# Performance work log

Hardware: AMD Instinct MI355X
Metric: run time of the kernel (lower is better)

Reference implementation:

```python
import jax, jax.numpy as jnp
import numpy as np

DIM = 384
HEADS = 8


def setup_inputs() -> dict:
    key = jax.random.key(0)
    ks = jax.random.split(key, 6)
    B, H, W = 8, 64, 64
    N, C = H * W, DIM
    s = 0.02  # init scale for weights
    return {
        "x": jax.random.normal(ks[0], (B, N, C), jnp.float32),
        # depthwise conv: OIHW with feature_group_count=C -> [C,1,3,3]
        "w_sr": jax.random.normal(ks[1], (C, 1, 3, 3), jnp.float32) * s,
        "b_sr": jax.random.normal(ks[2], (C,), jnp.float32) * s,
        "ln_g": jnp.ones((C,), jnp.float32),
        "ln_b": jnp.zeros((C,), jnp.float32),
        # linears stored [in, out] (torch stores [out,in]; random so equivalent)
        "w_qkv": jax.random.normal(ks[3], (C, 3 * C), jnp.float32) * s,
        "w_proj": jax.random.normal(ks[4], (C, C), jnp.float32) * s,
        "b_proj": jax.random.normal(ks[5], (C,), jnp.float32) * s,
        "H": 64,
        "W": 64,
    }


def reference(x, w_sr, b_sr, ln_g, ln_b, w_qkv, w_proj, b_proj, H, W):
    B, N, C = x.shape
    h = HEADS
    d = C // h
    shortcut = x

    # --- depthwise conv branch: sr(x) -> LN -> GELU -> residual add ---
    x_img = x.transpose(0, 2, 1).reshape(B, C, H, W)
    x_sr = jax.lax.conv_general_dilated(
        x_img, w_sr, window_strides=(1, 1), padding="SAME",
        dimension_numbers=("NCHW", "OIHW", "NCHW"), feature_group_count=C,
    ) + b_sr[None, :, None, None]
    x_sr = x_sr.reshape(B, C, N).transpose(0, 2, 1)  # [B, N, C]
    mu = x_sr.mean(-1, keepdims=True)
    var = x_sr.var(-1, keepdims=True)
    xn = (x_sr - mu) * jax.lax.rsqrt(var + 1e-5) * ln_g + ln_b
    x = x + jax.nn.gelu(xn, approximate=False)  # torch GELU is erf-based

    # --- linear attention ---
    qkv = (x @ w_qkv).reshape(B, N, 3, h, d)
    q = qkv[:, :, 0].transpose(0, 2, 1, 3)  # [B, h, N, d]
    k = qkv[:, :, 1].transpose(0, 2, 1, 3)
    v = qkv[:, :, 2].transpose(0, 2, 1, 3)
    q = jax.nn.softmax(q, axis=-2)  # softmax over sequence dim N
    k = jax.nn.softmax(k, axis=-1)  # softmax over head_dim
    ctx = jnp.einsum("bhnd,bhne->bhde", k, v)          # [B, h, d, d]
    attn = jnp.einsum("bhnd,bhde->bhne", q, ctx)       # [B, h, N, d]
    attn = attn.transpose(0, 2, 1, 3).reshape(B, N, C)

    out = attn @ w_proj + b_proj
    return out + shortcut
```

## Files before the change

### kernel.cpp

```cpp
#include <hip/hip_runtime.h>

typedef unsigned short u16;
typedef u16   u16x4  __attribute__((ext_vector_type(4)));
typedef u16   u16x8  __attribute__((ext_vector_type(8)));
typedef short short8 __attribute__((ext_vector_type(8)));
typedef float floatx4 __attribute__((ext_vector_type(4)));
typedef float f4     __attribute__((ext_vector_type(4)));

#define BB 8
#define NN 4096
#define CC 384

__device__ __forceinline__ u16 f2bf(float f){
  unsigned u = __float_as_uint(f);
  u += 0x7FFFu + ((u >> 16) & 1u);
  return (u16)(u >> 16);
}

__global__ __launch_bounds__(256) void k_prep(const float* __restrict__ wqkv, u16* __restrict__ WT)
{
  const int cg = blockIdx.x % 18;
  const int kg = blockIdx.x / 18;
  const int c0 = cg << 6, k0 = kg << 6;
  const int tid = threadIdx.x;
  __shared__ u16 t[64][72];
#pragma unroll
  for (int i = 0; i < 4; i++) {
    int idx = tid + (i << 8);
    int r = idx >> 4, c4 = (idx & 15) << 2;
    f4 v = *(const f4*)(wqkv + (size_t)(k0 + r) * 1152 + c0 + c4);
#pragma unroll
    for (int j = 0; j < 4; j++) t[c4 + j][r] = f2bf(v[j]);
  }
  __syncthreads();
#pragma unroll
  for (int i = 0; i < 2; i++) {
    int idx = tid + (i << 8);
    int c = idx >> 3, j = (idx & 7) << 3;
    *(u16x8*)(WT + (size_t)(c0 + c) * 384 + k0 + j) = *(const u16x8*)&t[c][j];
  }
}

__global__ __launch_bounds__(384) void k_conv_ln_gelu(
    const float* __restrict__ x, const float* __restrict__ w_sr, const float* __restrict__ b_sr,
    const float* __restrict__ ln_g, const float* __restrict__ ln_b, u16* __restrict__ xa16)
{
  const int blk = blockIdx.x;
  const int b = blk >> 9;
  const int hh = (blk >> 3) & 63;
  const int ww0 = (blk & 7) << 3;
  const int c = threadIdx.x;

  float wgt[9];
#pragma unroll
  for (int i = 0; i < 9; i++) wgt[i] = w_sr[c * 9 + i];
  const float lg = ln_g[c], lb = ln_b[c];
  const float bias = b_sr[c];

  float rowv[3][10];
#pragma unroll
  for (int r = 0; r < 3; r++) {
    int y = hh + r - 1;
    bool yok = (unsigned)y < 64u;
#pragma unroll
    for (int j = 0; j < 10; j++) {
      int xx = ww0 + j - 1;
      bool ok = yok && ((unsigned)xx < 64u);
      rowv[r][j] = ok ? x[((size_t)((b << 12) + (y << 6) + xx)) * CC + c] : 0.f;
    }
  }

  float acc[8];
#pragma unroll
  for (int p = 0; p < 8; p++) {
    float a = bias;
#pragma unroll
    for (int r = 0; r < 3; r++)
#pragma unroll
      for (int j = 0; j < 3; j++)
        a += rowv[r][p + j] * wgt[r * 3 + j];
    acc[p] = a;
  }

  __shared__ float ls1[6][8], ls2[6][8], mb[2][8];
  const int wid = threadIdx.x >> 6, lane = threadIdx.x & 63;
#pragma unroll
  for (int p = 0; p < 8; p++) {
    float s1 = acc[p], s2 = acc[p] * acc[p];
#pragma unroll
    for (int o = 32; o > 0; o >>= 1) { s1 += __shfl_down(s1, o); s2 += __shfl_down(s2, o); }
    if (lane == 0) { ls1[wid][p] = s1; ls2[wid][p] = s2; }
  }
  __syncthreads();
  if (threadIdx.x < 8) {
    int p = threadIdx.x;
    float a = 0.f, q = 0.f;
#pragma unroll
    for (int i = 0; i < 6; i++) { a += ls1[i][p]; q += ls2[i][p]; }
    float mean = a * (1.0f / CC);
    float var  = q * (1.0f / CC) - mean * mean;
    mb[0][p] = mean; mb[1][p] = rsqrtf(var + 1e-5f);
  }
  __syncthreads();
#pragma unroll
  for (int p = 0; p < 8; p++) {
    float xn = (acc[p] - mb[0][p]) * mb[1][p] * lg + lb;
    float g  = 0.5f * xn * (1.0f + erff(xn * 0.70710678118654752f));
    size_t pix = (size_t)(b << 12) + (hh << 6) + ww0 + p;
    xa16[pix * CC + c] = f2bf(rowv[1][p + 1] + g);
  }
}


__global__ __launch_bounds__(512) void k_kv(
    const u16* __restrict__ xa16, const u16* __restrict__ WT,
    u16* __restrict__ K16T, u16* __restrict__ V16T)
{
  const int rt = blockIdx.x;
  const int g  = blockIdx.y;
  const int b  = rt >> 6;
  const int n0 = rt << 6;
  const int tid = threadIdx.x;
  const int wv = tid >> 6, lane = tid & 63, l15 = lane & 15, quad = lane >> 4;
  const int wc = wv;

  __shared__ __attribute__((aligned(16))) u16 lA[2][64][40];
  __shared__ __attribute__((aligned(16))) u16 lB[2][384][40];

  const u16* Bbase = WT + (size_t)(384 + g * 384) * 384;
  const int rA = tid >> 2, cA = (tid & 3) << 3;

  floatx4 acc[12];
  const floatx4 z = {0.f, 0.f, 0.f, 0.f};
#pragma unroll
  for (int i = 0; i < 12; i++) acc[i] = z;

  if (tid < 256)
    *(u16x8*)&lA[0][rA][cA] = *(const u16x8*)(xa16 + (size_t)(n0 + rA) * 384 + cA);
#pragma unroll
  for (int i = 0; i < 3; i++) {
    int idx = tid + (i << 9);
    *(u16x8*)&lB[0][idx >> 2][(idx & 3) << 3] = *(const u16x8*)(Bbase + (size_t)(idx >> 2) * 384 + ((idx & 3) << 3));
  }
  __syncthreads();

  for (int t = 0; t < 12; t++) {
    const int cur = t & 1, nxt = cur ^ 1;
    u16x8 ra, rb[3];
    const bool pf = (t < 11);
    const int kn = (t + 1) << 5;
    if (pf) {
      if (tid < 256) ra = *(const u16x8*)(xa16 + (size_t)(n0 + rA) * 384 + kn + cA);
#pragma unroll
      for (int i = 0; i < 3; i++) {
        int idx = tid + (i << 9);
        rb[i] = *(const u16x8*)(Bbase + (size_t)(idx >> 2) * 384 + kn + ((idx & 3) << 3));
      }
    }
    short8 af[4], bf[3];
#pragma unroll
    for (int mi = 0; mi < 4; mi++) af[mi] = *(const short8*)&lA[cur][(mi << 4) + l15][quad << 3];
#pragma unroll
    for (int ni = 0; ni < 3; ni++) bf[ni] = *(const short8*)&lB[cur][wc * 48 + (ni << 4) + l15][quad << 3];
#pragma unroll
    for (int mi = 0; mi < 4; mi++)
#pragma unroll
      for (int ni = 0; ni < 3; ni++)
        acc[mi * 3 + ni] = __builtin_amdgcn_mfma_f32_16x16x32_bf16(af[mi], bf[ni], acc[mi * 3 + ni], 0, 0, 0);
    if (pf) {
      if (tid < 256) *(u16x8*)&lA[nxt][rA][cA] = ra;
#pragma unroll
      for (int i = 0; i < 3; i++) {
        int idx = tid + (i << 9);
        *(u16x8*)&lB[nxt][idx >> 2][(idx & 3) << 3] = rb[i];
      }
    }
    __syncthreads();
  }

  if (g == 0) {
#pragma unroll
    for (int mi = 0; mi < 4; mi++)
#pragma unroll
      for (int rr = 0; rr < 4; rr++) {
        float x0 = acc[mi * 3 + 0][rr], x1 = acc[mi * 3 + 1][rr], x2 = acc[mi * 3 + 2][rr];
        float m = fmaxf(fmaxf(x0, x1), x2);
#pragma unroll
        for (int o = 8; o >= 1; o >>= 1) m = fmaxf(m, __shfl_xor(m, o));
        float e0 = expf(x0 - m), e1 = expf(x1 - m), e2 = expf(x2 - m);
        float s = e0 + e1 + e2;
#pragma unroll
        for (int o = 8; o >= 1; o >>= 1) s += __shfl_xor(s, o);
        float inv = 1.0f / s;
        acc[mi * 3 + 0][rr] = e0 * inv; acc[mi * 3 + 1][rr] = e1 * inv; acc[mi * 3 + 2][rr] = e2 * inv;
      }
  }

  u16* dst = g ? V16T : K16T;
  const int nl = ((rt & 63) << 6) + (quad << 2);
#pragma unroll
  for (int mi = 0; mi < 4; mi++)
#pragma unroll
    for (int ni = 0; ni < 3; ni++) {
      int hd = wc * 48 + (ni << 4) + l15;
      u16x4 v4 = { f2bf(acc[mi * 3 + ni][0]), f2bf(acc[mi * 3 + ni][1]),
                   f2bf(acc[mi * 3 + ni][2]), f2bf(acc[mi * 3 + ni][3]) };
      *(u16x4*)(dst + ((size_t)b * 384 + hd) * 4096 + nl + (mi << 4)) = v4;
    }
}

__global__ __launch_bounds__(512) void k_qps(
    const u16* __restrict__ xa16, const u16* __restrict__ WT, float* __restrict__ S,
    u16* __restrict__ P16)
{
  const int bm = blockIdx.x;
  const int b = bm >> 6;
  const int n0 = bm << 6;
  const int tid = threadIdx.x;
  const int wv = tid >> 6, lane = tid & 63, l15 = lane & 15, quad = lane >> 4;
  const int wc = wv;

  __shared__ __attribute__((aligned(16))) u16 lA[2][64][40];
  __shared__ __attribute__((aligned(16))) u16 lB[2][384][40];

  const u16* Bbase = WT;
  const int rA = tid >> 2, cA = (tid & 3) << 3;

  floatx4 acc[12];
  const floatx4 z = {0.f, 0.f, 0.f, 0.f};
#pragma unroll
  for (int i = 0; i < 12; i++) acc[i] = z;

  if (tid < 256)
    *(u16x8*)&lA[0][rA][cA] = *(const u16x8*)(xa16 + (size_t)(n0 + rA) * 384 + cA);
#pragma unroll
  for (int i = 0; i < 3; i++) {
    int idx = tid + (i << 9);
    *(u16x8*)&lB[0][idx >> 2][(idx & 3) << 3] = *(const u16x8*)(Bbase + (size_t)(idx >> 2) * 384 + ((idx & 3) << 3));
  }
  __syncthreads();

  for (int t = 0; t < 12; t++) {
    const int cur = t & 1, nxt = cur ^ 1;
    u16x8 ra, rb[3];
    const bool pf = (t < 11);
    const int kn = (t + 1) << 5;
    if (pf) {
      if (tid < 256) ra = *(const u16x8*)(xa16 + (size_t)(n0 + rA) * 384 + kn + cA);
#pragma unroll
      for (int i = 0; i < 3; i++) {
        int idx = tid + (i << 9);
        rb[i] = *(const u16x8*)(Bbase + (size_t)(idx >> 2) * 384 + kn + ((idx & 3) << 3));
      }
    }
    short8 af[4], bf[3];
#pragma unroll
    for (int mi = 0; mi < 4; mi++) af[mi] = *(const short8*)&lA[cur][(mi << 4) + l15][quad << 3];
#pragma unroll
    for (int ni = 0; ni < 3; ni++) bf[ni] = *(const short8*)&lB[cur][wc * 48 + (ni << 4) + l15][quad << 3];
#pragma unroll
    for (int mi = 0; mi < 4; mi++)
#pragma unroll
      for (int ni = 0; ni < 3; ni++)
        acc[mi * 3 + ni] = __builtin_amdgcn_mfma_f32_16x16x32_bf16(af[mi], bf[ni], acc[mi * 3 + ni], 0, 0, 0);
    if (pf) {
      if (tid < 256) *(u16x8*)&lA[nxt][rA][cA] = ra;
#pragma unroll
      for (int i = 0; i < 3; i++) {
        int idx = tid + (i << 9);
        *(u16x8*)&lB[nxt][idx >> 2][(idx & 3) << 3] = rb[i];
      }
    }
    __syncthreads();
  }

#pragma unroll
  for (int ni = 0; ni < 3; ni++) {
    int col = wc * 48 + (ni << 4) + l15;
    float s = 0.f;
#pragma unroll
    for (int mi = 0; mi < 4; mi++) {
      int rowb = n0 + (mi << 4) + (quad << 2);
      float e0 = expf(acc[mi * 3 + ni][0]), e1 = expf(acc[mi * 3 + ni][1]);
      float e2 = expf(acc[mi * 3 + ni][2]), e3 = expf(acc[mi * 3 + ni][3]);
      P16[(size_t)(rowb + 0) * 384 + col] = f2bf(e0);
      P16[(size_t)(rowb + 1) * 384 + col] = f2bf(e1);
      P16[(size_t)(rowb + 2) * 384 + col] = f2bf(e2);
      P16[(size_t)(rowb + 3) * 384 + col] = f2bf(e3);
      s += e0 + e1 + e2 + e3;
    }
    s += __shfl_down(s, 32);
    s += __shfl_down(s, 16);
    if (lane < 16) atomicAdd(&S[b * 384 + wc * 48 + (ni << 4) + lane], s);
  }
}

__global__ __launch_bounds__(256) void k_ctx(
    const u16* __restrict__ K16T, const u16* __restrict__ V16T, float* __restrict__ ctx)
{
  const int bh = blockIdx.x;
  const int b = bh >> 3, h = bh & 7;
  const int n0 = blockIdx.y << 8;
  const int tid = threadIdx.x;
  const int wv = tid >> 6, lane = tid & 63, l15 = lane & 15, quad = lane >> 4;

  __shared__ __attribute__((aligned(16))) char smem[50688];
  u16 (*lkT)[264] = (u16(*)[264])smem;
  u16 (*lvT)[264] = (u16(*)[264])(smem + 25344);
  float (*pctx)[2304] = (float(*)[2304])smem;

#pragma unroll
  for (int i = 0; i < 6; i++) {
    int idx = tid + (i << 8);
    int d = idx >> 5, c8 = (idx & 31) << 3;
    *(u16x8*)&lkT[d][c8] = *(const u16x8*)(K16T + ((size_t)b * 384 + h * 48 + d) * 4096 + n0 + c8);
    *(u16x8*)&lvT[d][c8] = *(const u16x8*)(V16T + ((size_t)b * 384 + h * 48 + d) * 4096 + n0 + c8);
  }
  __syncthreads();

  floatx4 c2[9];
  const floatx4 z = {0.f, 0.f, 0.f, 0.f};
#pragma unroll
  for (int i = 0; i < 9; i++) c2[i] = z;
#pragma unroll
  for (int kk2 = 0; kk2 < 2; kk2++) {
    int rb = (wv << 6) + (kk2 << 5) + (quad << 3);
    short8 ak[3], av[3];
#pragma unroll
    for (int t = 0; t < 3; t++) {
      ak[t] = *(const short8*)&lkT[(t << 4) + l15][rb];
      av[t] = *(const short8*)&lvT[(t << 4) + l15][rb];
    }
#pragma unroll
    for (int dt = 0; dt < 3; dt++)
#pragma unroll
      for (int et = 0; et < 3; et++)
        c2[dt * 3 + et] = __builtin_amdgcn_mfma_f32_16x16x32_bf16(ak[dt], av[et], c2[dt * 3 + et], 0, 0, 0);
  }
  __syncthreads();

#pragma unroll
  for (int dt = 0; dt < 3; dt++)
#pragma unroll
    for (int et = 0; et < 3; et++)
#pragma unroll
      for (int rr = 0; rr < 4; rr++) {
        int d = (dt << 4) + (quad << 2) + rr;
        int e = (et << 4) + l15;
        pctx[wv][d * 48 + e] = c2[dt * 3 + et][rr];
      }
  __syncthreads();
#pragma unroll
  for (int i = 0; i < 9; i++) {
    int cell = tid + (i << 8);
    float s = pctx[0][cell] + pctx[1][cell] + pctx[2][cell] + pctx[3][cell];
    atomicAdd(&ctx[(size_t)bh * 2304 + cell], s);
  }
}

__global__ __launch_bounds__(256) void k_w2(
    const float* __restrict__ ctx, const float* __restrict__ S,
    const float* __restrict__ wp, u16* __restrict__ W2T)
{
  const int bh = blockIdx.x;
  const int b = bh >> 3, h = bh & 7;
  const int c0 = blockIdx.y << 7;
  const int tid = threadIdx.x;
  __shared__ float rs[48];
  __shared__ float c2[48][48];
  __shared__ float lwp[48][128];
  __shared__ u16 tr[128][48];
  if (tid < 48) rs[tid] = 1.0f / S[b * 384 + h * 48 + tid];
  __syncthreads();
#pragma unroll
  for (int i = 0; i < 9; i++) {
    int cell = tid + (i << 8);
    int d = cell / 48, e = cell - d * 48;
    c2[d][e] = ctx[(size_t)bh * 2304 + cell] * rs[d];
  }
#pragma unroll
  for (int i = 0; i < 24; i++) {
    int idx = tid + (i << 8);
    int e = idx >> 7, c = idx & 127;
    lwp[e][c] = wp[(size_t)(h * 48 + e) * 384 + c0 + c];
  }
  __syncthreads();
  const int c = tid & 127;
  const int dbase = tid >> 7;
#pragma unroll
  for (int it = 0; it < 24; it++) {
    int d = (it << 1) + dbase;
    float s = 0.f;
#pragma unroll
    for (int e = 0; e < 48; e++) s += c2[d][e] * lwp[e][c];
    tr[c][d] = f2bf(s);
  }
  __syncthreads();
  const int cc = tid >> 1, half = tid & 1;
#pragma unroll
  for (int i = 0; i < 3; i++) {
    u16x8 v = *(const u16x8*)&tr[cc][half * 24 + (i << 3)];
    *(u16x8*)(W2T + ((size_t)b * 384 + c0 + cc) * 384 + h * 48 + half * 24 + (i << 3)) = v;
  }
}

__global__ __launch_bounds__(512) void k_qproj(
    const u16* __restrict__ P16, const u16* __restrict__ W2T,
    const float* __restrict__ bias, const float* __restrict__ x, float* __restrict__ out)
{
  const int bm = blockIdx.x;
  const int b = bm >> 6;
  const int n0 = bm << 6;
  const int tid = threadIdx.x;
  const int wv = tid >> 6, lane = tid & 63, l15 = lane & 15, quad = lane >> 4;
  const int wc = wv;

  __shared__ __attribute__((aligned(16))) u16 lA[2][64][40];
  __shared__ __attribute__((aligned(16))) u16 lB[2][384][40];

  const u16* Bbase = W2T + (size_t)b * 384 * 384;
  const int rA = tid >> 2, cA = (tid & 3) << 3;

  floatx4 acc[12];
  const floatx4 z = {0.f, 0.f, 0.f, 0.f};
#pragma unroll
  for (int i = 0; i < 12; i++) acc[i] = z;

  if (tid < 256)
    *(u16x8*)&lA[0][rA][cA] = *(const u16x8*)(P16 + (size_t)(n0 + rA) * 384 + cA);
#pragma unroll
  for (int i = 0; i < 3; i++) {
    int idx = tid + (i << 9);
    *(u16x8*)&lB[0][idx >> 2][(idx & 3) << 3] = *(const u16x8*)(Bbase + (size_t)(idx >> 2) * 384 + ((idx & 3) << 3));
  }
  __syncthreads();

  for (int t = 0; t < 12; t++) {
    const int cur = t & 1, nxt = cur ^ 1;
    u16x8 ra, rb[3];
    const bool pf = (t < 11);
    const int kn = (t + 1) << 5;
    if (pf) {
      if (tid < 256) ra = *(const u16x8*)(P16 + (size_t)(n0 + rA) * 384 + kn + cA);
#pragma unroll
      for (int i = 0; i < 3; i++) {
        int idx = tid + (i << 9);
        rb[i] = *(const u16x8*)(Bbase + (size_t)(idx >> 2) * 384 + kn + ((idx & 3) << 3));
      }
    }
    short8 af[4], bf[3];
#pragma unroll
    for (int mi = 0; mi < 4; mi++) af[mi] = *(const short8*)&lA[cur][(mi << 4) + l15][quad << 3];
#pragma unroll
    for (int ni = 0; ni < 3; ni++) bf[ni] = *(const short8*)&lB[cur][wc * 48 + (ni << 4) + l15][quad << 3];
#pragma unroll
    for (int mi = 0; mi < 4; mi++)
#pragma unroll
      for (int ni = 0; ni < 3; ni++)
        acc[mi * 3 + ni] = __builtin_amdgcn_mfma_f32_16x16x32_bf16(af[mi], bf[ni], acc[mi * 3 + ni], 0, 0, 0);
    if (pf) {
      if (tid < 256) *(u16x8*)&lA[nxt][rA][cA] = ra;
#pragma unroll
      for (int i = 0; i < 3; i++) {
        int idx = tid + (i << 9);
        *(u16x8*)&lB[nxt][idx >> 2][(idx & 3) << 3] = rb[i];
      }
    }
    __syncthreads();
  }

#pragma unroll
  for (int ni = 0; ni < 3; ni++) {
    int col = wc * 48 + (ni << 4) + l15;
    float bc = bias[col];
#pragma unroll
    for (int mi = 0; mi < 4; mi++) {
#pragma unroll
      for (int rr = 0; rr < 4; rr++) {
        int row = n0 + (mi << 4) + (quad << 2) + rr;
        out[(size_t)row * 384 + col] = acc[mi * 3 + ni][rr] + bc + x[(size_t)row * 384 + col];
      }
    }
  }
}

extern "C" void kernel_launch(void* const* d_in, const int* in_sizes, int n_in,
                              void* d_out, int out_size, void* d_ws, size_t ws_size,
                              hipStream_t stream)
{
  const float* x      = (const float*)d_in[0];
  const float* w_sr   = (const float*)d_in[1];
  const float* b_sr   = (const float*)d_in[2];
  const float* ln_g   = (const float*)d_in[3];
  const float* ln_b   = (const float*)d_in[4];
  const float* w_qkv  = (const float*)d_in[5];
  const float* w_proj = (const float*)d_in[6];
  const float* b_proj = (const float*)d_in[7];
  float* out = (float*)d_out;

  float* S   = (float*)d_ws;
  float* ctx = (float*)((char*)d_ws + 12288);
  u16*   WT  = (u16*)((char*)d_ws + 602112);
  u16*   W2T = (u16*)((char*)d_ws + 1486848);
  u16*   xa16= (u16*)((char*)d_ws + 3846144);
  u16*   P16 = xa16;
  u16*   K16T= (u16*)d_out;
  u16*   V16T= (u16*)d_out + (size_t)8 * 384 * 4096;

  hipMemsetAsync(d_ws, 0, 602112, stream);

  k_prep<<<108, 256, 0, stream>>>(w_qkv, WT);
  k_conv_ln_gelu<<<BB * 512, 384, 0, stream>>>(x, w_sr, b_sr, ln_g, ln_b, xa16);
  k_kv<<<dim3(512, 2), 512, 0, stream>>>(xa16, WT, K16T, V16T);
  k_qps<<<512, 512, 0, stream>>>(xa16, WT, S, P16);
  k_ctx<<<dim3(64, 16), 256, 0, stream>>>(K16T, V16T, ctx);
  k_w2<<<dim3(64, 3), 256, 0, stream>>>(ctx, S, w_proj, W2T);
  k_qproj<<<512, 512, 0, stream>>>(P16, W2T, b_proj, x, out);
}
```

Baseline: 267.3 us.

## Fuse K/V and Q projection GEMMs into one kernel with LDS-staged transposed stores

Merges the separate K/V projection kernel and the Q-softmax-exp kernel into one kernel that loops over the three weight groups per 64-row tile. K and V are processed first, so Q's P16 output can overwrite xa16 (P16 aliases it) only after this block's K and V reads of those rows are done. K/V outputs are transposed through LDS so global stores become 16-byte coalesced, and shared-memory double buffering is replaced by single buffering with an extra barrier. This cuts a launch and improves the transposed stores, but it serializes the three GEMMs within a block and reduces grid parallelism from 1536 to 512 blocks.

Measured after the change: 282.0 us. 5.5% more time.

```diff
diff --git a/kernel.cpp b/kernel.cpp
--- a/kernel.cpp
+++ b/kernel.cpp
@@ -111,187 +111,136 @@
   }
 }
 
-
-__global__ __launch_bounds__(512) void k_kv(
-    const u16* __restrict__ xa16, const u16* __restrict__ WT,
-    u16* __restrict__ K16T, u16* __restrict__ V16T)
-{
-  const int rt = blockIdx.x;
-  const int g  = blockIdx.y;
-  const int b  = rt >> 6;
-  const int n0 = rt << 6;
-  const int tid = threadIdx.x;
-  const int wv = tid >> 6, lane = tid & 63, l15 = lane & 15, quad = lane >> 4;
-  const int wc = wv;
-
-  __shared__ __attribute__((aligned(16))) u16 lA[2][64][40];
-  __shared__ __attribute__((aligned(16))) u16 lB[2][384][40];
-
-  const u16* Bbase = WT + (size_t)(384 + g * 384) * 384;
-  const int rA = tid >> 2, cA = (tid & 3) << 3;
-
-  floatx4 acc[12];
-  const floatx4 z = {0.f, 0.f, 0.f, 0.f};
-#pragma unroll
-  for (int i = 0; i < 12; i++) acc[i] = z;
-
-  if (tid < 256)
-    *(u16x8*)&lA[0][rA][cA] = *(const u16x8*)(xa16 + (size_t)(n0 + rA) * 384 + cA);
-#pragma unroll
-  for (int i = 0; i < 3; i++) {
-    int idx = tid + (i << 9);
-    *(u16x8*)&lB[0][idx >> 2][(idx & 3) << 3] = *(const u16x8*)(Bbase + (size_t)(idx >> 2) * 384 + ((idx & 3) << 3));
-  }
-  __syncthreads();
-
-  for (int t = 0; t < 12; t++) {
-    const int cur = t & 1, nxt = cur ^ 1;
-    u16x8 ra, rb[3];
-    const bool pf = (t < 11);
-    const int kn = (t + 1) << 5;
-    if (pf) {
-      if (tid < 256) ra = *(const u16x8*)(xa16 + (size_t)(n0 + rA) * 384 + kn + cA);
-#pragma unroll
-      for (int i = 0; i < 3; i++) {
-        int idx = tid + (i << 9);
-        rb[i] = *(const u16x8*)(Bbase + (size_t)(idx >> 2) * 384 + kn + ((idx & 3) << 3));
-      }
-    }
-    short8 af[4], bf[3];
-#pragma unroll
-    for (int mi = 0; mi < 4; mi++) af[mi] = *(const short8*)&lA[cur][(mi << 4) + l15][quad << 3];
-#pragma unroll
-    for (int ni = 0; ni < 3; ni++) bf[ni] = *(const short8*)&lB[cur][wc * 48 + (ni << 4) + l15][quad << 3];
-#pragma unroll
-    for (int mi = 0; mi < 4; mi++)
-#pragma unroll
-      for (int ni = 0; ni < 3; ni++)
-        acc[mi * 3 + ni] = __builtin_amdgcn_mfma_f32_16x16x32_bf16(af[mi], bf[ni], acc[mi * 3 + ni], 0, 0, 0);
-    if (pf) {
-      if (tid < 256) *(u16x8*)&lA[nxt][rA][cA] = ra;
-#pragma unroll
-      for (int i = 0; i < 3; i++) {
-        int idx = tid + (i << 9);
-        *(u16x8*)&lB[nxt][idx >> 2][(idx & 3) << 3] = rb[i];
-      }
-    }
-    __syncthreads();
-  }
-
-  if (g == 0) {
-#pragma unroll
-    for (int mi = 0; mi < 4; mi++)
-#pragma unroll
-      for (int rr = 0; rr < 4; rr++) {
-        float x0 = acc[mi * 3 + 0][rr], x1 = acc[mi * 3 + 1][rr], x2 = acc[mi * 3 + 2][rr];
-        float m = fmaxf(fmaxf(x0, x1), x2);
-#pragma unroll
-        for (int o = 8; o >= 1; o >>= 1) m = fmaxf(m, __shfl_xor(m, o));
-        float e0 = expf(x0 - m), e1 = expf(x1 - m), e2 = expf(x2 - m);
-        float s = e0 + e1 + e2;
-#pragma unroll
-        for (int o = 8; o >= 1; o >>= 1) s += __shfl_xor(s, o);
-        float inv = 1.0f / s;
-        acc[mi * 3 + 0][rr] = e0 * inv; acc[mi * 3 + 1][rr] = e1 * inv; acc[mi * 3 + 2][rr] = e2 * inv;
-      }
-  }
-
-  u16* dst = g ? V16T : K16T;
-  const int nl = ((rt & 63) << 6) + (quad << 2);
-#pragma unroll
-  for (int mi = 0; mi < 4; mi++)
-#pragma unroll
-    for (int ni = 0; ni < 3; ni++) {
-      int hd = wc * 48 + (ni << 4) + l15;
-      u16x4 v4 = { f2bf(acc[mi * 3 + ni][0]), f2bf(acc[mi * 3 + ni][1]),
-                   f2bf(acc[mi * 3 + ni][2]), f2bf(acc[mi * 3 + ni][3]) };
-      *(u16x4*)(dst + ((size_t)b * 384 + hd) * 4096 + nl + (mi << 4)) = v4;
-    }
-}
-
-__global__ __launch_bounds__(512) void k_qps(
+__global__ __launch_bounds__(512) void k_qkv(
     const u16* __restrict__ xa16, const u16* __restrict__ WT, float* __restrict__ S,
-    u16* __restrict__ P16)
+    u16* __restrict__ K16T, u16* __restrict__ V16T, u16* __restrict__ P16)
 {
   const int bm = blockIdx.x;
-  const int b = bm >> 6;
+  const int b  = bm >> 6;
   const int n0 = bm << 6;
   const int tid = threadIdx.x;
   const int wv = tid >> 6, lane = tid & 63, l15 = lane & 15, quad = lane >> 4;
   const int wc = wv;
 
-  __shared__ __attribute__((aligned(16))) u16 lA[2][64][40];
-  __shared__ __attribute__((aligned(16))) u16 lB[2][384][40];
-
-  const u16* Bbase = WT;
+  __shared__ __attribute__((aligned(16))) char smem[55296];
+  u16 (*lA)[40] = (u16(*)[40])smem;
+  u16 (*lB)[40] = (u16(*)[40])(smem + 5120);
+  u16 (*tb)[72] = (u16(*)[72])smem;
+
   const int rA = tid >> 2, cA = (tid & 3) << 3;
-
-  floatx4 acc[12];
   const floatx4 z = {0.f, 0.f, 0.f, 0.f};
-#pragma unroll
-  for (int i = 0; i < 12; i++) acc[i] = z;
-
-  if (tid < 256)
-    *(u16x8*)&lA[0][rA][cA] = *(const u16x8*)(xa16 + (size_t)(n0 + rA) * 384 + cA);
-#pragma unroll
-  for (int i = 0; i < 3; i++) {
-    int idx = tid + (i << 9);
-    *(u16x8*)&lB[0][idx >> 2][(idx & 3) << 3] = *(const u16x8*)(Bbase + (size_t)(idx >> 2) * 384 + ((idx & 3) << 3));
-  }
-  __syncthreads();
-
-  for (int t = 0; t < 12; t++) {
-    const int cur = t & 1, nxt = cur ^ 1;
-    u16x8 ra, rb[3];
-    const bool pf = (t < 11);
-    const int kn = (t + 1) << 5;
-    if (pf) {
-      if (tid < 256) ra = *(const u16x8*)(xa16 + (size_t)(n0 + rA) * 384 + kn + cA);
-#pragma unroll
-      for (int i = 0; i < 3; i++) {
-        int idx = tid + (i << 9);
-        rb[i] = *(const u16x8*)(Bbase + (size_t)(idx >> 2) * 384 + kn + ((idx & 3) << 3));
-      }
-    }
-    short8 af[4], bf[3];
-#pragma unroll
-    for (int mi = 0; mi < 4; mi++) af[mi] = *(const short8*)&lA[cur][(mi << 4) + l15][quad << 3];
-#pragma unroll
-    for (int ni = 0; ni < 3; ni++) bf[ni] = *(const short8*)&lB[cur][wc * 48 + (ni << 4) + l15][quad << 3];
-#pragma unroll
-    for (int mi = 0; mi < 4; mi++)
-#pragma unroll
-      for (int ni = 0; ni < 3; ni++)
-        acc[mi * 3 + ni] = __builtin_amdgcn_mfma_f32_16x16x32_bf16(af[mi], bf[ni], acc[mi * 3 + ni], 0, 0, 0);
-    if (pf) {
-      if (tid < 256) *(u16x8*)&lA[nxt][rA][cA] = ra;
-#pragma unroll
-      for (int i = 0; i < 3; i++) {
-        int idx = tid + (i << 9);
-        *(u16x8*)&lB[nxt][idx >> 2][(idx & 3) << 3] = rb[i];
-      }
+
+#pragma unroll 1
+  for (int gi = 0; gi < 3; gi++) {
+    const int g = (gi == 0) ? 1 : (gi == 1) ? 2 : 0;
+    const u16* Bbase = WT + (size_t)g * 384 * 384;
+
+    floatx4 acc[12];
+#pragma unroll
+    for (int i = 0; i < 12; i++) acc[i] = z;
+
+    if (tid < 256)
+      *(u16x8*)&lA[rA][cA] = *(const u16x8*)(xa16 + (size_t)(n0 + rA) * 384 + cA);
+#pragma unroll
+    for (int i = 0; i < 3; i++) {
+      int idx = tid + (i << 9);
+      *(u16x8*)&lB[idx >> 2][(idx & 3) << 3] = *(const u16x8*)(Bbase + (size_t)(idx >> 2) * 384 + ((idx & 3) << 3));
     }
     __syncthreads();
-  }
-
-#pragma unroll
-  for (int ni = 0; ni < 3; ni++) {
-    int col = wc * 48 + (ni << 4) + l15;
-    float s = 0.f;
-#pragma unroll
-    for (int mi = 0; mi < 4; mi++) {
-      int rowb = n0 + (mi << 4) + (quad << 2);
-      float e0 = expf(acc[mi * 3 + ni][0]), e1 = expf(acc[mi * 3 + ni][1]);
-      float e2 = expf(acc[mi * 3 + ni][2]), e3 = expf(acc[mi * 3 + ni][3]);
-      P16[(size_t)(rowb + 0) * 384 + col] = f2bf(e0);
-      P16[(size_t)(rowb + 1) * 384 + col] = f2bf(e1);
-      P16[(size_t)(rowb + 2) * 384 + col] = f2bf(e2);
-      P16[(size_t)(rowb + 3) * 384 + col] = f2bf(e3);
-      s += e0 + e1 + e2 + e3;
-    }
-    s += __shfl_down(s, 32);
-    s += __shfl_down(s, 16);
-    if (lane < 16) atomicAdd(&S[b * 384 + wc * 48 + (ni << 4) + lane], s);
+
+    for (int t = 0; t < 12; t++) {
+      u16x8 ra, rb[3];
+      const bool pf = (t < 11);
+      const int kn = (t + 1) << 5;
+      if (pf) {
+        if (tid < 256) ra = *(const u16x8*)(xa16 + (size_t)(n0 + rA) * 384 + kn + cA);
+#pragma unroll
+        for (int i = 0; i < 3; i++) {
+          int idx = tid + (i << 9);
+          rb[i] = *(const u16x8*)(Bbase + (size_t)(idx >> 2) * 384 + kn + ((idx & 3) << 3));
+        }
+      }
+      short8 af[4], bf[3];
+#pragma unroll
+      for (int mi = 0; mi < 4; mi++) af[mi] = *(const short8*)&lA[(mi << 4) + l15][quad << 3];
+#pragma unroll
+      for (int ni = 0; ni < 3; ni++) bf[ni] = *(const short8*)&lB[wc * 48 + (ni << 4) + l15][quad << 3];
+#pragma unroll
+      for (int mi = 0; mi < 4; mi++)
+#pragma unroll
+        for (int ni = 0; ni < 3; ni++)
+          acc[mi * 3 + ni] = __builtin_amdgcn_mfma_f32_16x16x32_bf16(af[mi], bf[ni], acc[mi * 3 + ni], 0, 0, 0);
+      __syncthreads();
+      if (pf) {
+        if (tid < 256) *(u16x8*)&lA[rA][cA] = ra;
+#pragma unroll
+        for (int i = 0; i < 3; i++) {
+          int idx = tid + (i << 9);
+          *(u16x8*)&lB[idx >> 2][(idx & 3) << 3] = rb[i];
+        }
+      }
+      __syncthreads();
+    }
+
+    if (g == 1) {
+#pragma unroll
+      for (int mi = 0; mi < 4; mi++)
+#pragma unroll
+        for (int rr = 0; rr < 4; rr++) {
+          float x0 = acc[mi * 3 + 0][rr], x1 = acc[mi * 3 + 1][rr], x2 = acc[mi * 3 + 2][rr];
+          float m = fmaxf(fmaxf(x0, x1), x2);
+#pragma unroll
+          for (int o = 8; o >= 1; o >>= 1) m = fmaxf(m, __shfl_xor(m, o));
+          float e0 = expf(x0 - m), e1 = expf(x1 - m), e2 = expf(x2 - m);
+          float s = e0 + e1 + e2;
+#pragma unroll
+          for (int o = 8; o >= 1; o >>= 1) s += __shfl_xor(s, o);
+          float inv = 1.0f / s;
+          acc[mi * 3 + 0][rr] = e0 * inv; acc[mi * 3 + 1][rr] = e1 * inv; acc[mi * 3 + 2][rr] = e2 * inv;
+        }
+    }
+
+    if (g == 0) {
+#pragma unroll
+      for (int ni = 0; ni < 3; ni++) {
+        int col = wc * 48 + (ni << 4) + l15;
+        float s = 0.f;
+#pragma unroll
+        for (int mi = 0; mi < 4; mi++) {
+          int rowb = n0 + (mi << 4) + (quad << 2);
+          float e0 = expf(acc[mi * 3 + ni][0]), e1 = expf(acc[mi * 3 + ni][1]);
+          float e2 = expf(acc[mi * 3 + ni][2]), e3 = expf(acc[mi * 3 + ni][3]);
+          P16[(size_t)(rowb + 0) * 384 + col] = f2bf(e0);
+          P16[(size_t)(rowb + 1) * 384 + col] = f2bf(e1);
+          P16[(size_t)(rowb + 2) * 384 + col] = f2bf(e2);
+          P16[(size_t)(rowb + 3) * 384 + col] = f2bf(e3);
+          s += e0 + e1 + e2 + e3;
+        }
+        s += __shfl_down(s, 32);
+        s += __shfl_down(s, 16);
+        if (lane < 16) atomicAdd(&S[b * 384 + wc * 48 + (ni << 4) + lane], s);
+      }
+    } else {
+#pragma unroll
+      for (int mi = 0; mi < 4; mi++)
+#pragma unroll
+        for (int ni = 0; ni < 3; ni++) {
+          int hd = wc * 48 + (ni << 4) + l15;
+          u16x4 v4 = { f2bf(acc[mi * 3 + ni][0]), f2bf(acc[mi * 3 + ni][1]),
+                       f2bf(acc[mi * 3 + ni][2]), f2bf(acc[mi * 3 + ni][3]) };
+          *(u16x4*)&tb[hd][(mi << 4) + (quad << 2)] = v4;
+        }
+      __syncthreads();
+      u16* dst = (g == 1) ? K16T : V16T;
+      const int nl0 = (bm & 63) << 6;
+#pragma unroll
+      for (int i = 0; i < 6; i++) {
+        int cid = tid + (i << 9);
+        int hd = cid >> 3, off = (cid & 7) << 3;
+        *(u16x8*)(dst + ((size_t)b * 384 + hd) * 4096 + nl0 + off) = *(const u16x8*)&tb[hd][off];
+      }
+      __syncthreads();
+    }
   }
 }
 
@@ -511,8 +460,7 @@
 
   k_prep<<<108, 256, 0, stream>>>(w_qkv, WT);
   k_conv_ln_gelu<<<BB * 512, 384, 0, stream>>>(x, w_sr, b_sr, ln_g, ln_b, xa16);
-  k_kv<<<dim3(512, 2), 512, 0, stream>>>(xa16, WT, K16T, V16T);
-  k_qps<<<512, 512, 0, stream>>>(xa16, WT, S, P16);
+  k_qkv<<<512, 512, 0, stream>>>(xa16, WT, S, K16T, V16T, P16);
   k_ctx<<<dim3(64, 16), 256, 0, stream>>>(K16T, V16T, ctx);
   k_w2<<<dim3(64, 3), 256, 0, stream>>>(ctx, S, w_proj, W2T);
   k_qproj<<<512, 512, 0, stream>>>(P16, W2T, b_proj, x, out);
```

## Use direct global-to-LDS loads with XOR-swizzled unpadded tiles in GEMM kernels

Applied to the files above, without the earlier changes.

Replaces the register-staged global→LDS copy in the three GEMM kernels (k_kv, k_qps, k_qproj) with global_load_lds, which writes straight into shared memory. This removes the VGPR round trip and the separate LDS stores. The padded 40-wide tiles become 32-wide tiles with an XOR swizzle on the 8-element column groups, which keeps LDS reads conflict-free and reduces LDS footprint. The risk is correctness: each lane's LDS destination is implied by the instruction, and the swizzle has to match on the read side.

After: 265.0 us. Within noise of the previous version (-0.9%).

```diff
diff --git a/kernel.cpp b/kernel.cpp
--- a/kernel.cpp
+++ b/kernel.cpp
@@ -6,6 +6,9 @@
 typedef short short8 __attribute__((ext_vector_type(8)));
 typedef float floatx4 __attribute__((ext_vector_type(4)));
 typedef float f4     __attribute__((ext_vector_type(4)));
+
+typedef const __attribute__((address_space(1))) unsigned gu32;
+typedef __attribute__((address_space(3))) unsigned lu32;
 
 #define BB 8
 #define NN 4096
@@ -124,57 +127,50 @@
   const int wv = tid >> 6, lane = tid & 63, l15 = lane & 15, quad = lane >> 4;
   const int wc = wv;
 
-  __shared__ __attribute__((aligned(16))) u16 lA[2][64][40];
-  __shared__ __attribute__((aligned(16))) u16 lB[2][384][40];
+  __shared__ __attribute__((aligned(16))) u16 lA[2][64][32];
+  __shared__ __attribute__((aligned(16))) u16 lB[2][384][32];
 
   const u16* Bbase = WT + (size_t)(384 + g * 384) * 384;
-  const int rA = tid >> 2, cA = (tid & 3) << 3;
+  const int sw8 = (quad ^ ((l15 >> 1) & 3)) << 3;
 
   floatx4 acc[12];
   const floatx4 z = {0.f, 0.f, 0.f, 0.f};
 #pragma unroll
   for (int i = 0; i < 12; i++) acc[i] = z;
 
-  if (tid < 256)
-    *(u16x8*)&lA[0][rA][cA] = *(const u16x8*)(xa16 + (size_t)(n0 + rA) * 384 + cA);
-#pragma unroll
-  for (int i = 0; i < 3; i++) {
-    int idx = tid + (i << 9);
-    *(u16x8*)&lB[0][idx >> 2][(idx & 3) << 3] = *(const u16x8*)(Bbase + (size_t)(idx >> 2) * 384 + ((idx & 3) << 3));
-  }
+  auto stage = [&](int bi, int k0) {
+    if (wv < 4) {
+      int cl = (wv << 4) + (lane >> 2);
+      int sc = ((lane & 3) ^ ((cl >> 1) & 3)) << 3;
+      __builtin_amdgcn_global_load_lds((gu32*)(xa16 + (size_t)(n0 + cl) * 384 + k0 + sc),
+                                       (lu32*)&lA[bi][wv << 4][0], 16, 0, 0);
+    }
+#pragma unroll
+    for (int i = 0; i < 3; i++) {
+      int j = wv * 3 + i;
+      int cl = (j << 4) + (lane >> 2);
+      int sc = ((lane & 3) ^ ((cl >> 1) & 3)) << 3;
+      __builtin_amdgcn_global_load_lds((gu32*)(Bbase + (size_t)cl * 384 + k0 + sc),
+                                       (lu32*)&lB[bi][j << 4][0], 16, 0, 0);
+    }
+  };
+
+  stage(0, 0);
   __syncthreads();
 
   for (int t = 0; t < 12; t++) {
-    const int cur = t & 1, nxt = cur ^ 1;
-    u16x8 ra, rb[3];
-    const bool pf = (t < 11);
-    const int kn = (t + 1) << 5;
-    if (pf) {
-      if (tid < 256) ra = *(const u16x8*)(xa16 + (size_t)(n0 + rA) * 384 + kn + cA);
-#pragma unroll
-      for (int i = 0; i < 3; i++) {
-        int idx = tid + (i << 9);
-        rb[i] = *(const u16x8*)(Bbase + (size_t)(idx >> 2) * 384 + kn + ((idx & 3) << 3));
-      }
-    }
+    const int cur = t & 1;
+    if (t < 11) stage(cur ^ 1, (t + 1) << 5);
     short8 af[4], bf[3];
 #pragma unroll
-    for (int mi = 0; mi < 4; mi++) af[mi] = *(const short8*)&lA[cur][(mi << 4) + l15][quad << 3];
-#pragma unroll
-    for (int ni = 0; ni < 3; ni++) bf[ni] = *(const short8*)&lB[cur][wc * 48 + (ni << 4) + l15][quad << 3];
+    for (int mi = 0; mi < 4; mi++) af[mi] = *(const short8*)&lA[cur][(mi << 4) + l15][sw8];
+#pragma unroll
+    for (int ni = 0; ni < 3; ni++) bf[ni] = *(const short8*)&lB[cur][wc * 48 + (ni << 4) + l15][sw8];
 #pragma unroll
     for (int mi = 0; mi < 4; mi++)
 #pragma unroll
       for (int ni = 0; ni < 3; ni++)
         acc[mi * 3 + ni] = __builtin_amdgcn_mfma_f32_16x16x32_bf16(af[mi], bf[ni], acc[mi * 3 + ni], 0, 0, 0);
-    if (pf) {
-      if (tid < 256) *(u16x8*)&lA[nxt][rA][cA] = ra;
-#pragma unroll
-      for (int i = 0; i < 3; i++) {
-        int idx = tid + (i << 9);
-        *(u16x8*)&lB[nxt][idx >> 2][(idx & 3) << 3] = rb[i];
-      }
-    }
     __syncthreads();
   }
 
@@ -220,57 +216,50 @@
   const int wv = tid >> 6, lane = tid & 63, l15 = lane & 15, quad = lane >> 4;
   const int wc = wv;
 
-  __shared__ __attribute__((aligned(16))) u16 lA[2][64][40];
-  __shared__ __attribute__((aligned(16))) u16 lB[2][384][40];
+  __shared__ __attribute__((aligned(16))) u16 lA[2][64][32];
+  __shared__ __attribute__((aligned(16))) u16 lB[2][384][32];
 
   const u16* Bbase = WT;
-  const int rA = tid >> 2, cA = (tid & 3) << 3;
+  const int sw8 = (quad ^ ((l15 >> 1) & 3)) << 3;
 
   floatx4 acc[12];
   const floatx4 z = {0.f, 0.f, 0.f, 0.f};
 #pragma unroll
   for (int i = 0; i < 12; i++) acc[i] = z;
 
-  if (tid < 256)
-    *(u16x8*)&lA[0][rA][cA] = *(const u16x8*)(xa16 + (size_t)(n0 + rA) * 384 + cA);
-#pragma unroll
-  for (int i = 0; i < 3; i++) {
-    int idx = tid + (i << 9);
-    *(u16x8*)&lB[0][idx >> 2][(idx & 3) << 3] = *(const u16x8*)(Bbase + (size_t)(idx >> 2) * 384 + ((idx & 3) << 3));
-  }
+  auto stage = [&](int bi, int k0) {
+    if (wv < 4) {
+      int cl = (wv << 4) + (lane >> 2);
+      int sc = ((lane & 3) ^ ((cl >> 1) & 3)) << 3;
+      __builtin_amdgcn_global_load_lds((gu32*)(xa16 + (size_t)(n0 + cl) * 384 + k0 + sc),
+                                       (lu32*)&lA[bi][wv << 4][0], 16, 0, 0);
+    }
+#pragma unroll
+    for (int i = 0; i < 3; i++) {
+      int j = wv * 3 + i;
+      int cl = (j << 4) + (lane >> 2);
+      int sc = ((lane & 3) ^ ((cl >> 1) & 3)) << 3;
+      __builtin_amdgcn_global_load_lds((gu32*)(Bbase + (size_t)cl * 384 + k0 + sc),
+                                       (lu32*)&lB[bi][j << 4][0], 16, 0, 0);
+    }
+  };
+
+  stage(0, 0);
   __syncthreads();
 
   for (int t = 0; t < 12; t++) {
-    const int cur = t & 1, nxt = cur ^ 1;
-    u16x8 ra, rb[3];
-    const bool pf = (t < 11);
-    const int kn = (t + 1) << 5;
-    if (pf) {
-      if (tid < 256) ra = *(const u16x8*)(xa16 + (size_t)(n0 + rA) * 384 + kn + cA);
-#pragma unroll
-      for (int i = 0; i < 3; i++) {
-        int idx = tid + (i << 9);
-        rb[i] = *(const u16x8*)(Bbase + (size_t)(idx >> 2) * 384 + kn + ((idx & 3) << 3));
-      }
-    }
+    const int cur = t & 1;
+    if (t < 11) stage(cur ^ 1, (t + 1) << 5);
     short8 af[4], bf[3];
 #pragma unroll
-    for (int mi = 0; mi < 4; mi++) af[mi] = *(const short8*)&lA[cur][(mi << 4) + l15][quad << 3];
-#pragma unroll
-    for (int ni = 0; ni < 3; ni++) bf[ni] = *(const short8*)&lB[cur][wc * 48 + (ni << 4) + l15][quad << 3];
+    for (int mi = 0; mi < 4; mi++) af[mi] = *(const short8*)&lA[cur][(mi << 4) + l15][sw8];
+#pragma unroll
+    for (int ni = 0; ni < 3; ni++) bf[ni] = *(const short8*)&lB[cur][wc * 48 + (ni << 4) + l15][sw8];
 #pragma unroll
     for (int mi = 0; mi < 4; mi++)
 #pragma unroll
       for (int ni = 0; ni < 3; ni++)
         acc[mi * 3 + ni] = __builtin_amdgcn_mfma_f32_16x16x32_bf16(af[mi], bf[ni], acc[mi * 3 + ni], 0, 0, 0);
-    if (pf) {
-      if (tid < 256) *(u16x8*)&lA[nxt][rA][cA] = ra;
-#pragma unroll
-      for (int i = 0; i < 3; i++) {
-        int idx = tid + (i << 9);
-        *(u16x8*)&lB[nxt][idx >> 2][(idx & 3) << 3] = rb[i];
-      }
-    }
     __syncthreads();
   }
 
@@ -415,57 +404,50 @@
   const int wv = tid >> 6, lane = tid & 63, l15 = lane & 15, quad = lane >> 4;
   const int wc = wv;
 
-  __shared__ __attribute__((aligned(16))) u16 lA[2][64][40];
-  __shared__ __attribute__((aligned(16))) u16 lB[2][384][40];
+  __shared__ __attribute__((aligned(16))) u16 lA[2][64][32];
+  __shared__ __attribute__((aligned(16))) u16 lB[2][384][32];
 
   const u16* Bbase = W2T + (size_t)b * 384 * 384;
-  const int rA = tid >> 2, cA = (tid & 3) << 3;
+  const int sw8 = (quad ^ ((l15 >> 1) & 3)) << 3;
 
   floatx4 acc[12];
   const floatx4 z = {0.f, 0.f, 0.f, 0.f};
 #pragma unroll
   for (int i = 0; i < 12; i++) acc[i] = z;
 
-  if (tid < 256)
-    *(u16x8*)&lA[0][rA][cA] = *(const u16x8*)(P16 + (size_t)(n0 + rA) * 384 + cA);
-#pragma unroll
-  for (int i = 0; i < 3; i++) {
-    int idx = tid + (i << 9);
-    *(u16x8*)&lB[0][idx >> 2][(idx & 3) << 3] = *(const u16x8*)(Bbase + (size_t)(idx >> 2) * 384 + ((idx & 3) << 3));
-  }
+  auto stage = [&](int bi, int k0) {
+    if (wv < 4) {
+      int cl = (wv << 4) + (lane >> 2);
+      int sc = ((lane & 3) ^ ((cl >> 1) & 3)) << 3;
+      __builtin_amdgcn_global_load_lds((gu32*)(P16 + (size_t)(n0 + cl) * 384 + k0 + sc),
+                                       (lu32*)&lA[bi][wv << 4][0], 16, 0, 0);
+    }
+#pragma unroll
+    for (int i = 0; i < 3; i++) {
+      int j = wv * 3 + i;
+      int cl = (j << 4) + (lane >> 2);
+      int sc = ((lane & 3) ^ ((cl >> 1) & 3)) << 3;
+      __builtin_amdgcn_global_load_lds((gu32*)(Bbase + (size_t)cl * 384 + k0 + sc),
+                                       (lu32*)&lB[bi][j << 4][0], 16, 0, 0);
+    }
+  };
+
+  stage(0, 0);
   __syncthreads();
 
   for (int t = 0; t < 12; t++) {
-    const int cur = t & 1, nxt = cur ^ 1;
-    u16x8 ra, rb[3];
-    const bool pf = (t < 11);
-    const int kn = (t + 1) << 5;
-    if (pf) {
-      if (tid < 256) ra = *(const u16x8*)(P16 + (size_t)(n0 + rA) * 384 + kn + cA);
-#pragma unroll
-      for (int i = 0; i < 3; i++) {
-        int idx = tid + (i << 9);
-        rb[i] = *(const u16x8*)(Bbase + (size_t)(idx >> 2) * 384 + kn + ((idx & 3) << 3));
-      }
-    }
+    const int cur = t & 1;
+    if (t < 11) stage(cur ^ 1, (t + 1) << 5);
     short8 af[4], bf[3];
 #pragma unroll
-    for (int mi = 0; mi < 4; mi++) af[mi] = *(const short8*)&lA[cur][(mi << 4) + l15][quad << 3];
-#pragma unroll
-    for (int ni = 0; ni < 3; ni++) bf[ni] = *(const short8*)&lB[cur][wc * 48 + (ni << 4) + l15][quad << 3];
+    for (int mi = 0; mi < 4; mi++) af[mi] = *(const short8*)&lA[cur][(mi << 4) + l15][sw8];
+#pragma unroll
+    for (int ni = 0; ni < 3; ni++) bf[ni] = *(const short8*)&lB[cur][wc * 48 + (ni << 4) + l15][sw8];
 #pragma unroll
     for (int mi = 0; mi < 4; mi++)
 #pragma unroll
       for (int ni = 0; ni < 3; ni++)
         acc[mi * 3 + ni] = __builtin_amdgcn_mfma_f32_16x16x32_bf16(af[mi], bf[ni], acc[mi * 3 + ni], 0, 0, 0);
-    if (pf) {
-      if (tid < 256) *(u16x8*)&lA[nxt][rA][cA] = ra;
-#pragma unroll
-      for (int i = 0; i < 3; i++) {
-        int idx = tid + (i << 9);
-        *(u16x8*)&lB[nxt][idx >> 2][(idx & 3) << 3] = rb[i];
-      }
-    }
     __syncthreads();
   }
 
```
